# Performance work log

Measured on AMD Instinct MI355X. Metric: run time of the kernel, lower is better.

Reference implementation:

```python
import jax, jax.numpy as jnp
import numpy as np

N = 40000          # nodes
E = 320000         # edges
IN_DIM = 16
H = 64             # num_hidden
EDGE_DIM = 8
NUM_FILTERS = 2
SCALE = 3
T = 4              # num_layers (time steps)
DC = EDGE_DIM * NUM_FILTERS   # edge_dim_cat = 16
HC = H + DC                   # concat(h, efeat_p) dim
S1 = SCALE - 1


def setup_inputs() -> dict:
    key = jax.random.key(0)
    ks = jax.random.split(key, 24)
    def nrm(k, shape, fan):
        return jax.random.normal(k, shape, dtype=jnp.float32) / np.float32(np.sqrt(fan))
    return {
        "inputs": jax.random.normal(ks[0], (N, IN_DIM), dtype=jnp.float32),
        "e_feats": jax.random.normal(ks[1], (E, EDGE_DIM, T), dtype=jnp.float32),
        "rain0": jax.random.uniform(ks[2], (N, T), dtype=jnp.float32),
        "src": jax.random.randint(ks[3], (E,), 0, N),
        "dst": jax.random.randint(ks[4], (E,), 0, N),
        # embedding (no bias)
        "W_emb": nrm(ks[5], (IN_DIM, H), IN_DIM),
        # ST_EIConvSPGRAD (IN) layers, one per scale step: edge MLP split into per-source terms
        "Win_hs": nrm(ks[6], (S1, H, H), 2 * H + EDGE_DIM + 1),
        "Win_hd": nrm(ks[7], (S1, H, H), 2 * H + EDGE_DIM + 1),
        "Win_e": nrm(ks[8], (S1, EDGE_DIM, H), 2 * H + EDGE_DIM + 1),
        "Win_r": nrm(ks[9], (S1, H), 2 * H + EDGE_DIM + 1),
        # ST_EIConvProp (PROP) layers (edge-feature propagation, out_on=False)
        "Wp_hs": nrm(ks[10], (S1, H, DC), 2 * H + DC + 1),
        "Wp_hd": nrm(ks[11], (S1, H, DC), 2 * H + DC + 1),
        "Wp_e": nrm(ks[12], (S1, DC, DC), 2 * H + DC + 1),
        "Wp_r": nrm(ks[13], (S1, DC), 2 * H + DC + 1),
        # ST_EIConvProp OUT layer (out_on=True) on concatenated node features
        "Wo_hs": nrm(ks[14], (HC, H), 2 * HC + EDGE_DIM + 1),
        "Wo_hd": nrm(ks[15], (HC, H), 2 * HC + EDGE_DIM + 1),
        "Wo_e": nrm(ks[16], (EDGE_DIM, H), 2 * HC + EDGE_DIM + 1),
        "Wo_r": nrm(ks[17], (H,), 2 * HC + EDGE_DIM + 1),
        "W_rain": nrm(ks[18], (H,), H),
    }


def reference(inputs, e_feats, rain0, src, dst,
              W_emb, Win_hs, Win_hd, Win_e, Win_r,
              Wp_hs, Wp_hd, Wp_e, Wp_r,
              Wo_hs, Wo_hd, Wo_e, Wo_r, W_rain):
    relu = jax.nn.relu
    agg = lambda m: jax.ops.segment_sum(m, dst, num_segments=N)

    def in_layer(s, h, ef, rain):
        # per-edge message: MLP over [h_src, h_dst, efeat, rain_src], split matmuls avoid concat
        m = relu(h[src] @ Win_hs[s] + h[dst] @ Win_hd[s]
                 + ef @ Win_e[s] + rain[src, None] * Win_r[s][None, :])
        return relu(agg(m))                      # [N, H]

    def prop_layer(s, h, ef, rain):
        # ef is edge-level [E, DC] on first call, node-level [N, DC] thereafter (gather at src)
        ef_e = ef if ef.shape[0] == E else ef[src]
        m = relu(h[src] @ Wp_hs[s] + h[dst] @ Wp_hd[s]
                 + ef_e @ Wp_e[s] + rain[src, None] * Wp_r[s][None, :])
        return agg(m)                            # [N, DC]

    def out_layer(h_out, ef, rain):
        m = relu(h_out[src] @ Wo_hs + h_out[dst] @ Wo_hd
                 + ef @ Wo_e + rain[src, None] * Wo_r[None, :])
        h_new = relu(agg(m))                     # [N, H]
        rain_out = h_new @ W_rain                # [N]
        return rain_out, h_new

    def step(h, ef_t, rain_t, first):
        for s in range(S1):
            h = in_layer(s, h, ef_t, rain_t)
        ef_exp = jnp.tile(ef_t, (1, NUM_FILTERS))        # [E, DC]
        p = prop_layer(0, h, ef_exp, rain_t)
        # faithful quirk: first time step re-applies PROP[0] (range starts at 0);
        # later steps start at 1
        rng = range(S1) if first else range(1, S1)
        for s in rng:
            p = prop_layer(s, h, p, rain_t)
        h_out = jnp.concatenate([h, p], axis=1)          # [N, HC]
        rain_m, h = out_layer(h_out, ef_t, rain_t)
        return rain_m, h

    h = inputs @ W_emb                                   # [N, H]
    rains = []
    for t in range(T):
        rain_m, h = step(h, e_feats[:, :, t], rain0[:, t], first=(t == 0))
        rains.append(rain_m)
    return jnp.stack(rains, axis=1)                      # [N, T]
```

## Files before the change

kernel.cpp:

```cpp
#include <hip/hip_runtime.h>

#define NN 40000
#define NE 320000
#define TT 4
#define SCAN_CHUNK 1024
#define NBLK_SCAN ((NN + SCAN_CHUNK - 1) / SCAN_CHUNK)

typedef unsigned short u16;

__device__ __forceinline__ float bcastf(float v, int k) {
    return __builtin_bit_cast(float, __builtin_amdgcn_readlane(__builtin_bit_cast(int, v), k));
}
__device__ __forceinline__ int bcasti(int v, int k) {
    return __builtin_amdgcn_readlane(v, k);
}
__device__ __forceinline__ float b2f(u16 u) {
    return __builtin_bit_cast(float, (unsigned)u << 16);
}
__device__ __forceinline__ u16 f2b(float f) {
    unsigned x = __builtin_bit_cast(unsigned, f);
    unsigned r = x + 0x7fffu + ((x >> 16) & 1u);
    return (u16)(r >> 16);
}
__device__ __forceinline__ float lo16(unsigned u) {
    return __builtin_bit_cast(float, u << 16);
}
__device__ __forceinline__ float hi16(unsigned u) {
    return __builtin_bit_cast(float, u & 0xffff0000u);
}

__global__ void emb_kernel(const float* __restrict__ x, const float* __restrict__ W,
                           u16* __restrict__ h) {
    int i = blockIdx.x * blockDim.x + threadIdx.x;
    if (i >= NN * 64) return;
    int n = i >> 6, j = i & 63;
    float acc = 0.f;
#pragma unroll
    for (int k = 0; k < 16; ++k) acc = fmaf(x[n * 16 + k], W[k * 64 + j], acc);
    h[i] = f2b(acc);
}

__global__ void wfold_kernel(const float* __restrict__ We, float* __restrict__ Wf) {
    int i = threadIdx.x;
    if (i < 128) Wf[i] = We[i] + We[i + 128];
}

__global__ void hist_kernel(const int* __restrict__ dst, int* __restrict__ deg) {
    int e = blockIdx.x * blockDim.x + threadIdx.x;
    if (e < NE) atomicAdd(&deg[dst[e]], 1);
}

__global__ void scan1_kernel(const int* __restrict__ deg, int* __restrict__ bsum) {
    __shared__ int sdata[256];
    int b = blockIdx.x, t = threadIdx.x;
    int base = b * SCAN_CHUNK;
    int sum = 0;
    for (int i = t; i < SCAN_CHUNK; i += 256) {
        int idx = base + i;
        sum += (idx < NN) ? deg[idx] : 0;
    }
    sdata[t] = sum;
    __syncthreads();
    for (int off = 128; off > 0; off >>= 1) {
        if (t < off) sdata[t] += sdata[t + off];
        __syncthreads();
    }
    if (t == 0) bsum[b] = sdata[0];
}

__global__ void scan2_kernel(const int* __restrict__ bsum, int* __restrict__ boff,
                             int* __restrict__ rowptr) {
    if (threadIdx.x == 0) {
        int acc = 0;
        for (int i = 0; i < NBLK_SCAN; ++i) {
            boff[i] = acc;
            acc += bsum[i];
        }
        rowptr[NN] = NE;
    }
}

__global__ void scan3_kernel(const int* __restrict__ deg, const int* __restrict__ boff,
                             int* __restrict__ rowptr, int* __restrict__ cursor) {
    __shared__ int ss[256];
    int b = blockIdx.x, t = threadIdx.x;
    int base = b * SCAN_CHUNK + t * 4;
    int v[4], s = 0;
#pragma unroll
    for (int q = 0; q < 4; ++q) {
        int idx = base + q;
        v[q] = (idx < NN) ? deg[idx] : 0;
        s += v[q];
    }
    ss[t] = s;
    __syncthreads();
    for (int off = 1; off < 256; off <<= 1) {
        int add = (t >= off) ? ss[t - off] : 0;
        __syncthreads();
        ss[t] += add;
        __syncthreads();
    }
    int excl = boff[b] + ss[t] - s;
#pragma unroll
    for (int q = 0; q < 4; ++q) {
        int idx = base + q;
        if (idx < NN) {
            rowptr[idx] = excl;
            cursor[idx] = excl;
        }
        excl += v[q];
    }
}

__global__ void scatter_kernel(const int* __restrict__ src, const int* __restrict__ dst,
                               int* __restrict__ cursor, int* __restrict__ perm,
                               int* __restrict__ srcp) {
    int e = blockIdx.x * blockDim.x + threadIdx.x;
    if (e >= NE) return;
    int d = dst[e];
    int pos = atomicAdd(&cursor[d], 1);
    perm[pos] = e;
    srcp[pos] = src[e];
}

__global__ void efperm_all_kernel(const float* __restrict__ ef, const int* __restrict__ perm,
                                  u16* __restrict__ out) {
    int pos = blockIdx.x * blockDim.x + threadIdx.x;
    if (pos >= NE) return;
    int e = perm[pos];
    const float4* e4 = reinterpret_cast<const float4*>(ef) + (size_t)e * 8;
#pragma unroll
    for (int k = 0; k < 8; ++k) {
        float4 v = e4[k];
        out[0 * (size_t)NE * 8 + pos * 8 + k] = f2b(v.x);
        out[1 * (size_t)NE * 8 + pos * 8 + k] = f2b(v.y);
        out[2 * (size_t)NE * 8 + pos * 8 + k] = f2b(v.z);
        out[3 * (size_t)NE * 8 + pos * 8 + k] = f2b(v.w);
    }
}

__global__ void efperm_one_kernel(const float* __restrict__ ef, const int* __restrict__ perm,
                                  int t, u16* __restrict__ out) {
    int i = blockIdx.x * blockDim.x + threadIdx.x;
    if (i >= NE * 8) return;
    int pos = i >> 3, k = i & 7;
    int e = perm[pos];
    out[i] = f2b(ef[((size_t)e * 8 + k) * 4 + t]);
}

__global__ __launch_bounds__(256) void node_ab_kernel(
    const u16* __restrict__ X1, int relu1,
    const float* __restrict__ X2, int d2,
    const float* __restrict__ Whs, const float* __restrict__ Whd,
    const float* __restrict__ rain, const float* __restrict__ Wr,
    u16* __restrict__ A, u16* __restrict__ B) {
    extern __shared__ float sW[];
    const int dtot = 64 + d2;
    float* sWs = sW;
    float* sWd = sW + (dtot << 6);
    for (int i = threadIdx.x; i < (dtot << 6); i += 256) {
        sWs[i] = Whs[i];
        sWd[i] = Whd[i];
    }
    __syncthreads();
    const int lane = threadIdx.x & 63;
    const int wid = (blockIdx.x << 2) + (threadIdx.x >> 6);
    const int n0 = wid << 3;
    const float wr = Wr[lane];
    float xv[8], aa[8], bb[8];
#pragma unroll
    for (int p = 0; p < 8; ++p) {
        float x = b2f(__builtin_nontemporal_load(&X1[(size_t)(n0 + p) * 64 + lane]));
        xv[p] = relu1 ? fmaxf(x, 0.f) : x;
        aa[p] = rain[(n0 + p) * TT] * wr;
        bb[p] = 0.f;
    }
#pragma unroll 16
    for (int k = 0; k < 64; ++k) {
        float ws = sWs[(k << 6) + lane];
        float wd = sWd[(k << 6) + lane];
#pragma unroll
        for (int p = 0; p < 8; ++p) {
            float xk = bcastf(xv[p], k);
            aa[p] = fmaf(xk, ws, aa[p]);
            bb[p] = fmaf(xk, wd, bb[p]);
        }
    }
    if (d2) {
#pragma unroll
        for (int p = 0; p < 8; ++p) xv[p] = X2[(n0 + p) * 16 + (lane & 15)];
#pragma unroll
        for (int k = 0; k < 16; ++k) {
            float ws = sWs[((64 + k) << 6) + lane];
            float wd = sWd[((64 + k) << 6) + lane];
#pragma unroll
            for (int p = 0; p < 8; ++p) {
                float xk = bcastf(xv[p], k);
                aa[p] = fmaf(xk, ws, aa[p]);
                bb[p] = fmaf(xk, wd, bb[p]);
            }
        }
    }
#pragma unroll
    for (int p = 0; p < 8; ++p) {
        A[(size_t)(n0 + p) * 64 + lane] = f2b(aa[p]);
        B[(size_t)(n0 + p) * 64 + lane] = f2b(bb[p]);
    }
}

__global__ __launch_bounds__(256) void node_p_all(
    const u16* __restrict__ X,
    const float* __restrict__ Whs, const float* __restrict__ Whd,
    const float* __restrict__ rain, const float* __restrict__ Wr,
    float* __restrict__ Ap0, float* __restrict__ Bp0,
    float* __restrict__ Ap1, float* __restrict__ Bp1) {
    __shared__ float sX[64 * 68];
    __shared__ float sW[4][1024];
    for (int i = threadIdx.x; i < 1024; i += 256) {
        sW[0][i] = Whs[i];
        sW[1][i] = Whd[i];
        sW[2][i] = Whs[1024 + i];
        sW[3][i] = Whd[1024 + i];
    }
    const int n0 = blockIdx.x << 6;
    for (int i = threadIdx.x; i < 512; i += 256) {
        int row = i >> 3, col = (i & 7) << 3;
        uint4 v = *reinterpret_cast<const uint4*>(&X[(size_t)(n0 + row) * 64 + col]);
        float* d = &sX[row * 68 + col];
        d[0] = fmaxf(lo16(v.x), 0.f);
        d[1] = fmaxf(hi16(v.x), 0.f);
        d[2] = fmaxf(lo16(v.y), 0.f);
        d[3] = fmaxf(hi16(v.y), 0.f);
        d[4] = fmaxf(lo16(v.z), 0.f);
        d[5] = fmaxf(hi16(v.z), 0.f);
        d[6] = fmaxf(lo16(v.w), 0.f);
        d[7] = fmaxf(hi16(v.w), 0.f);
    }
    __syncthreads();
    const int j = threadIdx.x & 15;
    const int nl0 = threadIdx.x >> 4;
    const float wr0 = Wr[j], wr1 = Wr[16 + j];
    float a0[4], b0[4], a1[4], b1[4];
#pragma unroll
    for (int q = 0; q < 4; ++q) {
        float rn = rain[(n0 + nl0 + (q << 4)) * TT];
        a0[q] = rn * wr0;
        a1[q] = rn * wr1;
        b0[q] = 0.f;
        b1[q] = 0.f;
    }
#pragma unroll 4
    for (int k = 0; k < 64; ++k) {
        float wa0 = sW[0][(k << 4) + j], wb0 = sW[1][(k << 4) + j];
        float wa1 = sW[2][(k << 4) + j], wb1 = sW[3][(k << 4) + j];
#pragma unroll
        for (int q = 0; q < 4; ++q) {
            float x = sX[(nl0 + (q << 4)) * 68 + k];
            a0[q] = fmaf(x, wa0, a0[q]);
            b0[q] = fmaf(x, wb0, b0[q]);
            a1[q] = fmaf(x, wa1, a1[q]);
            b1[q] = fmaf(x, wb1, b1[q]);
        }
    }
#pragma unroll
    for (int q = 0; q < 4; ++q) {
        int n = n0 + nl0 + (q << 4);
        Ap0[n * 16 + j] = a0[q];
        Bp0[n * 16 + j] = b0[q];
        Ap1[n * 16 + j] = a1[q];
        Bp1[n * 16 + j] = b1[q];
    }
}

__global__ __launch_bounds__(256) void edge64_csr(
    const u16* __restrict__ A, const u16* __restrict__ B,
    const u16* __restrict__ efp, const float* __restrict__ We,
    const int* __restrict__ rowptr, const int* __restrict__ srcp,
    u16* __restrict__ agg, const float* __restrict__ Wrain,
    float* __restrict__ out, int t) {
    const int lane = threadIdx.x & 63;
    const int n = (blockIdx.x << 2) + (threadIdx.x >> 6);
    const float w0 = We[lane], w1 = We[64 + lane];
    const float w2 = We[128 + lane], w3 = We[192 + lane];
    const float w4 = We[256 + lane], w5 = We[320 + lane];
    const float w6 = We[384 + lane], w7 = We[448 + lane];
    const int beg = rowptr[n], end = rowptr[n + 1];
    const int deg = end - beg;
    int sv = 0;
    if (beg + lane < NE) sv = srcp[beg + lane];
    const float b = b2f(__builtin_nontemporal_load(&B[(size_t)n * 64 + lane]));
    const uint4* ef4 = reinterpret_cast<const uint4*>(efp);
    float acc = 0.f;
    for (int k0 = 0; k0 < deg; k0 += 4) {
        u16 av[4];
        uint4 ev[4];
#pragma unroll
        for (int i = 0; i < 4; ++i) {
            int kk = k0 + i;
            if (kk > deg - 1) kk = deg - 1;
            int s = (kk < 64) ? bcasti(sv, kk) : srcp[beg + kk];
            av[i] = A[(size_t)s * 64 + lane];
            ev[i] = ef4[(size_t)(beg + kk)];
        }
#pragma unroll
        for (int i = 0; i < 4; ++i) {
            if (k0 + i < deg) {
                float m = b2f(av[i]) + b;
                m = fmaf(lo16(ev[i].x), w0, m);
                m = fmaf(hi16(ev[i].x), w1, m);
                m = fmaf(lo16(ev[i].y), w2, m);
                m = fmaf(hi16(ev[i].y), w3, m);
                m = fmaf(lo16(ev[i].z), w4, m);
                m = fmaf(hi16(ev[i].z), w5, m);
                m = fmaf(lo16(ev[i].w), w6, m);
                m = fmaf(hi16(ev[i].w), w7, m);
                acc += fmaxf(m, 0.f);
            }
        }
    }
    __builtin_nontemporal_store(f2b(acc), &agg[(size_t)n * 64 + lane]);
    if (out) {
        float r = fmaxf(acc, 0.f) * Wrain[lane];
#pragma unroll
        for (int off = 32; off > 0; off >>= 1) r += __shfl_down(r, off);
        if (lane == 0) out[n * TT + t] = r;
    }
}

__global__ __launch_bounds__(256) void edge16_csr(
    const float* __restrict__ G, const float* __restrict__ Bp,
    const u16* __restrict__ efp, const float* __restrict__ Wf, int has_ef,
    const float* __restrict__ ApN, const float* __restrict__ WeN,
    float* __restrict__ PeSN, int has_epi,
    const int* __restrict__ rowptr, const int* __restrict__ srcp,
    float* __restrict__ pout) {
    const int lane = threadIdx.x & 63;
    const int g = lane >> 4, j = lane & 15;
    float w[8];
    if (has_ef) {
#pragma unroll
        for (int k = 0; k < 8; ++k) w[k] = Wf[k * 16 + j];
    }
    const int wid = (blockIdx.x * 256 + threadIdx.x) >> 6;
    const int n = (wid << 2) + g;
    const int beg = rowptr[n], end = rowptr[n + 1];
    const float b = Bp[n * 16 + j];
    const uint4* ef4 = reinterpret_cast<const uint4*>(efp);
    float acc = 0.f;
    int s_nxt = (beg + 1 < end) ? srcp[beg + 1] : 0;
    float av = (beg < end) ? G[srcp[beg] * 16 + j] : 0.f;
    for (int pos = beg; pos < end; ++pos) {
        float avc = av;
        int s_nn = (pos + 2 < end) ? srcp[pos + 2] : 0;
        if (pos + 1 < end) av = G[s_nxt * 16 + j];
        s_nxt = s_nn;
        float m = avc + b;
        if (has_ef) {
            uint4 ev = ef4[(size_t)pos];
            m = fmaf(lo16(ev.x), w[0], m);
            m = fmaf(hi16(ev.x), w[1], m);
            m = fmaf(lo16(ev.y), w[2], m);
            m = fmaf(hi16(ev.y), w[3], m);
            m = fmaf(lo16(ev.z), w[4], m);
            m = fmaf(hi16(ev.z), w[5], m);
            m = fmaf(lo16(ev.w), w[6], m);
            m = fmaf(hi16(ev.w), w[7], m);
        }
        acc += fmaxf(m, 0.f);
    }
    if (pout) pout[n * 16 + j] = acc;
    if (has_epi) {
        float pe = ApN[n * 16 + j];
        const int gbase = lane & 48;
#pragma unroll
        for (int k = 0; k < 16; ++k) {
            float pk = __shfl(acc, gbase + k);
            pe = fmaf(pk, WeN[k * 16 + j], pe);
        }
        PeSN[n * 16 + j] = pe;
    }
}

extern "C" void kernel_launch(void* const* d_in, const int* in_sizes, int n_in,
                              void* d_out, int out_size, void* d_ws, size_t ws_size,
                              hipStream_t stream) {
    (void)in_sizes; (void)n_in; (void)out_size;
    const float* inputs = (const float*)d_in[0];
    const float* e_feats = (const float*)d_in[1];
    const float* rain0 = (const float*)d_in[2];
    const int* src = (const int*)d_in[3];
    const int* dst = (const int*)d_in[4];
    const float* W_emb = (const float*)d_in[5];
    const float* Win_hs = (const float*)d_in[6];
    const float* Win_hd = (const float*)d_in[7];
    const float* Win_e = (const float*)d_in[8];
    const float* Win_r = (const float*)d_in[9];
    const float* Wp_hs = (const float*)d_in[10];
    const float* Wp_hd = (const float*)d_in[11];
    const float* Wp_e = (const float*)d_in[12];
    const float* Wp_r = (const float*)d_in[13];
    const float* Wo_hs = (const float*)d_in[14];
    const float* Wo_hd = (const float*)d_in[15];
    const float* Wo_e = (const float*)d_in[16];
    const float* Wo_r = (const float*)d_in[17];
    const float* W_rain = (const float*)d_in[18];
    float* out = (float*)d_out;

    const size_t NF64 = (size_t)NN * 64;
    const size_t NF16 = (size_t)NN * 16;
    const size_t EF = (size_t)NE * 8;

    char* base = (char*)d_ws;
    auto alloc = [&](size_t bytes) -> char* {
        char* p = base;
        base += (bytes + 255) & ~(size_t)255;
        return p;
    };

    const size_t fixed = 5 * NF64 * 2 + 7 * NF16 * 4 +
                         (2 * (size_t)NE + 3 * (size_t)NN + 200) * 4 + 64 * 256;
    const bool big = ws_size >= fixed + 4 * EF * 2;

    u16 *A16, *B16, *aggA16, *aggB16, *aggO16, *efp16;
    float *Ap0, *Bp0, *Ap1, *Bp1, *PeSa, *PeSb, *pbuf, *Wfold;
    A16 = (u16*)alloc(NF64 * 2);
    B16 = (u16*)alloc(NF64 * 2);
    aggA16 = (u16*)alloc(NF64 * 2);
    aggB16 = (u16*)alloc(NF64 * 2);
    aggO16 = (u16*)alloc(NF64 * 2);
    Ap0 = (float*)alloc(NF16 * 4);
    Bp0 = (float*)alloc(NF16 * 4);
    Ap1 = (float*)alloc(NF16 * 4);
    Bp1 = (float*)alloc(NF16 * 4);
    PeSa = (float*)alloc(NF16 * 4);
    PeSb = (float*)alloc(NF16 * 4);
    pbuf = (float*)alloc(NF16 * 4);
    Wfold = (float*)alloc(128 * 4);
    efp16 = (u16*)alloc((big ? 4 * EF : EF) * 2);
    int* srcp = (int*)alloc(NE * 4);
    int* perm = (int*)alloc(NE * 4);
    int* rowptr = (int*)alloc((NN + 1) * 4);
    int* deg = (int*)alloc(NN * 4);
    int* cursor = (int*)alloc(NN * 4);
    int* bsum = (int*)alloc(64 * 4);
    int* boff = (int*)alloc(64 * 4);
    u16* hemb = aggO16;

    hipMemsetAsync(deg, 0, NN * sizeof(int), stream);
    hist_kernel<<<(NE + 255) / 256, 256, 0, stream>>>(dst, deg);
    scan1_kernel<<<NBLK_SCAN, 256, 0, stream>>>(deg, bsum);
    scan2_kernel<<<1, 64, 0, stream>>>(bsum, boff, rowptr);
    scan3_kernel<<<NBLK_SCAN, 256, 0, stream>>>(deg, boff, rowptr, cursor);
    scatter_kernel<<<(NE + 255) / 256, 256, 0, stream>>>(src, dst, cursor, perm, srcp);
    if (big)
        efperm_all_kernel<<<(NE + 255) / 256, 256, 0, stream>>>(e_feats, perm, efp16);

    emb_kernel<<<(NN * 64 + 255) / 256, 256, 0, stream>>>(inputs, W_emb, hemb);
    wfold_kernel<<<1, 128, 0, stream>>>(Wp_e, Wfold);

    for (int t = 0; t < TT; ++t) {
        const float* rain = rain0 + t;
        const u16* eft = big ? (efp16 + (size_t)t * EF) : efp16;
        if (!big)
            efperm_one_kernel<<<(NE * 8 + 255) / 256, 256, 0, stream>>>(e_feats, perm, t, efp16);

        node_ab_kernel<<<1250, 256, 64 * 64 * 2 * sizeof(float), stream>>>(
            aggO16, (t > 0) ? 1 : 0, nullptr, 0,
            Win_hs, Win_hd, rain, Win_r, A16, B16);
        edge64_csr<<<10000, 256, 0, stream>>>(A16, B16, eft, Win_e, rowptr, srcp, aggA16,
                                              nullptr, nullptr, 0);

        node_ab_kernel<<<1250, 256, 64 * 64 * 2 * sizeof(float), stream>>>(
            aggA16, 1, nullptr, 0, Win_hs + 4096, Win_hd + 4096, rain, Win_r + 64, A16, B16);
        edge64_csr<<<10000, 256, 0, stream>>>(A16, B16, eft, Win_e + 512, rowptr, srcp, aggB16,
                                              nullptr, nullptr, 0);

        node_p_all<<<625, 256, 0, stream>>>(aggB16, Wp_hs, Wp_hd, rain, Wp_r,
                                            Ap0, Bp0, Ap1, Bp1);

        if (t == 0) {
            edge16_csr<<<2500, 256, 0, stream>>>(Ap0, Bp0, eft, Wfold, 1,
                                                 Ap0, Wp_e, PeSa, 1,
                                                 rowptr, srcp, nullptr);
            edge16_csr<<<2500, 256, 0, stream>>>(PeSa, Bp0, nullptr, nullptr, 0,
                                                 Ap1, Wp_e + 256, PeSb, 1,
                                                 rowptr, srcp, nullptr);
            edge16_csr<<<2500, 256, 0, stream>>>(PeSb, Bp1, nullptr, nullptr, 0,
                                                 nullptr, nullptr, nullptr, 0,
                                                 rowptr, srcp, pbuf);
        } else {
            edge16_csr<<<2500, 256, 0, stream>>>(Ap0, Bp0, eft, Wfold, 1,
                                                 Ap1, Wp_e + 256, PeSa, 1,
                                                 rowptr, srcp, nullptr);
            edge16_csr<<<2500, 256, 0, stream>>>(PeSa, Bp1, nullptr, nullptr, 0,
                                                 nullptr, nullptr, nullptr, 0,
                                                 rowptr, srcp, pbuf);
        }

        node_ab_kernel<<<1250, 256, 80 * 64 * 2 * sizeof(float), stream>>>(
            aggB16, 1, pbuf, 16, Wo_hs, Wo_hd, rain, Wo_r, A16, B16);
        edge64_csr<<<10000, 256, 0, stream>>>(A16, B16, eft, Wo_e, rowptr, srcp, aggO16,
                                              W_rain, out, t);
    }
}
```

Measured before the change: 953.2 us.

## Process nodes in descending-degree order in CSR edge kernels

Adds a degree histogram, scan and scatter that build a node ordering sorted by in-degree, descending and capped at 64. The edge64 and edge16 CSR kernels then pick their node through this order, so waves in a block and neighbouring blocks see similar degrees. This is meant to reduce divergence and load imbalance from random degree variation. The cost is an extra indirection per wave, three setup kernels, and worse locality when writing node outputs.

```diff
diff --git a/kernel.cpp b/kernel.cpp
--- a/kernel.cpp
+++ b/kernel.cpp
@@ -121,6 +121,34 @@
     int pos = atomicAdd(&cursor[d], 1);
     perm[pos] = e;
     srcp[pos] = src[e];
+}
+
+__global__ void dhist_kernel(const int* __restrict__ rowptr, int* __restrict__ dh) {
+    int n = blockIdx.x * blockDim.x + threadIdx.x;
+    if (n >= NN) return;
+    int d = rowptr[n + 1] - rowptr[n];
+    if (d > 64) d = 64;
+    atomicAdd(&dh[64 - d], 1);
+}
+
+__global__ void dscan_kernel(const int* __restrict__ dh, int* __restrict__ dcur) {
+    if (threadIdx.x == 0) {
+        int a = 0;
+        for (int i = 0; i < 65; ++i) {
+            dcur[i] = a;
+            a += dh[i];
+        }
+    }
+}
+
+__global__ void dscatter_kernel(const int* __restrict__ rowptr, int* __restrict__ dcur,
+                                int* __restrict__ order) {
+    int n = blockIdx.x * blockDim.x + threadIdx.x;
+    if (n >= NN) return;
+    int d = rowptr[n + 1] - rowptr[n];
+    if (d > 64) d = 64;
+    int pos = atomicAdd(&dcur[64 - d], 1);
+    order[pos] = n;
 }
 
 __global__ void efperm_all_kernel(const float* __restrict__ ef, const int* __restrict__ perm,
@@ -276,10 +304,11 @@
     const u16* __restrict__ A, const u16* __restrict__ B,
     const u16* __restrict__ efp, const float* __restrict__ We,
     const int* __restrict__ rowptr, const int* __restrict__ srcp,
+    const int* __restrict__ order,
     u16* __restrict__ agg, const float* __restrict__ Wrain,
     float* __restrict__ out, int t) {
     const int lane = threadIdx.x & 63;
-    const int n = (blockIdx.x << 2) + (threadIdx.x >> 6);
+    const int n = order[(blockIdx.x << 2) + (threadIdx.x >> 6)];
     const float w0 = We[lane], w1 = We[64 + lane];
     const float w2 = We[128 + lane], w3 = We[192 + lane];
     const float w4 = We[256 + lane], w5 = We[320 + lane];
@@ -333,6 +362,7 @@
     const float* __restrict__ ApN, const float* __restrict__ WeN,
     float* __restrict__ PeSN, int has_epi,
     const int* __restrict__ rowptr, const int* __restrict__ srcp,
+    const int* __restrict__ order,
     float* __restrict__ pout) {
     const int lane = threadIdx.x & 63;
     const int g = lane >> 4, j = lane & 15;
@@ -342,7 +372,7 @@
         for (int k = 0; k < 8; ++k) w[k] = Wf[k * 16 + j];
     }
     const int wid = (blockIdx.x * 256 + threadIdx.x) >> 6;
-    const int n = (wid << 2) + g;
+    const int n = order[(wid << 2) + g];
     const int beg = rowptr[n], end = rowptr[n + 1];
     const float b = Bp[n * 16 + j];
     const uint4* ef4 = reinterpret_cast<const uint4*>(efp);
@@ -418,7 +448,7 @@
     };
 
     const size_t fixed = 5 * NF64 * 2 + 7 * NF16 * 4 +
-                         (2 * (size_t)NE + 3 * (size_t)NN + 200) * 4 + 64 * 256;
+                         (2 * (size_t)NE + 4 * (size_t)NN + 400) * 4 + 64 * 256;
     const bool big = ws_size >= fixed + 4 * EF * 2;
 
     u16 *A16, *B16, *aggA16, *aggB16, *aggO16, *efp16;
@@ -442,16 +472,23 @@
     int* rowptr = (int*)alloc((NN + 1) * 4);
     int* deg = (int*)alloc(NN * 4);
     int* cursor = (int*)alloc(NN * 4);
+    int* order = (int*)alloc(NN * 4);
     int* bsum = (int*)alloc(64 * 4);
     int* boff = (int*)alloc(64 * 4);
+    int* dh = (int*)alloc(65 * 4);
+    int* dcur = (int*)alloc(65 * 4);
     u16* hemb = aggO16;
 
     hipMemsetAsync(deg, 0, NN * sizeof(int), stream);
+    hipMemsetAsync(dh, 0, 65 * sizeof(int), stream);
     hist_kernel<<<(NE + 255) / 256, 256, 0, stream>>>(dst, deg);
     scan1_kernel<<<NBLK_SCAN, 256, 0, stream>>>(deg, bsum);
     scan2_kernel<<<1, 64, 0, stream>>>(bsum, boff, rowptr);
     scan3_kernel<<<NBLK_SCAN, 256, 0, stream>>>(deg, boff, rowptr, cursor);
     scatter_kernel<<<(NE + 255) / 256, 256, 0, stream>>>(src, dst, cursor, perm, srcp);
+    dhist_kernel<<<(NN + 255) / 256, 256, 0, stream>>>(rowptr, dh);
+    dscan_kernel<<<1, 64, 0, stream>>>(dh, dcur);
+    dscatter_kernel<<<(NN + 255) / 256, 256, 0, stream>>>(rowptr, dcur, order);
     if (big)
         efperm_all_kernel<<<(NE + 255) / 256, 256, 0, stream>>>(e_feats, perm, efp16);
 
@@ -467,13 +504,13 @@
         node_ab_kernel<<<1250, 256, 64 * 64 * 2 * sizeof(float), stream>>>(
             aggO16, (t > 0) ? 1 : 0, nullptr, 0,
             Win_hs, Win_hd, rain, Win_r, A16, B16);
-        edge64_csr<<<10000, 256, 0, stream>>>(A16, B16, eft, Win_e, rowptr, srcp, aggA16,
-                                              nullptr, nullptr, 0);
+        edge64_csr<<<10000, 256, 0, stream>>>(A16, B16, eft, Win_e, rowptr, srcp, order,
+                                              aggA16, nullptr, nullptr, 0);
 
         node_ab_kernel<<<1250, 256, 64 * 64 * 2 * sizeof(float), stream>>>(
             aggA16, 1, nullptr, 0, Win_hs + 4096, Win_hd + 4096, rain, Win_r + 64, A16, B16);
-        edge64_csr<<<10000, 256, 0, stream>>>(A16, B16, eft, Win_e + 512, rowptr, srcp, aggB16,
-                                              nullptr, nullptr, 0);
+        edge64_csr<<<10000, 256, 0, stream>>>(A16, B16, eft, Win_e + 512, rowptr, srcp, order,
+                                              aggB16, nullptr, nullptr, 0);
 
         node_p_all<<<625, 256, 0, stream>>>(aggB16, Wp_hs, Wp_hd, rain, Wp_r,
                                             Ap0, Bp0, Ap1, Bp1);
@@ -481,25 +518,25 @@
         if (t == 0) {
             edge16_csr<<<2500, 256, 0, stream>>>(Ap0, Bp0, eft, Wfold, 1,
                                                  Ap0, Wp_e, PeSa, 1,
-                                                 rowptr, srcp, nullptr);
+                                                 rowptr, srcp, order, nullptr);
             edge16_csr<<<2500, 256, 0, stream>>>(PeSa, Bp0, nullptr, nullptr, 0,
                                                  Ap1, Wp_e + 256, PeSb, 1,
-                                                 rowptr, srcp, nullptr);
+                                                 rowptr, srcp, order, nullptr);
             edge16_csr<<<2500, 256, 0, stream>>>(PeSb, Bp1, nullptr, nullptr, 0,
                                                  nullptr, nullptr, nullptr, 0,
-                                                 rowptr, srcp, pbuf);
+                                                 rowptr, srcp, order, pbuf);
         } else {
             edge16_csr<<<2500, 256, 0, stream>>>(Ap0, Bp0, eft, Wfold, 1,
                                                  Ap1, Wp_e + 256, PeSa, 1,
-                                                 rowptr, srcp, nullptr);
+                                                 rowptr, srcp, order, nullptr);
             edge16_csr<<<2500, 256, 0, stream>>>(PeSa, Bp1, nullptr, nullptr, 0,
                                                  nullptr, nullptr, nullptr, 0,
-                                                 rowptr, srcp, pbuf);
+                                                 rowptr, srcp, order, pbuf);
         }
 
         node_ab_kernel<<<1250, 256, 80 * 64 * 2 * sizeof(float), stream>>>(
             aggB16, 1, pbuf, 16, Wo_hs, Wo_hd, rain, Wo_r, A16, B16);
-        edge64_csr<<<10000, 256, 0, stream>>>(A16, B16, eft, Wo_e, rowptr, srcp, aggO16,
-                                              W_rain, out, t);
-    }
-}
+        edge64_csr<<<10000, 256, 0, stream>>>(A16, B16, eft, Wo_e, rowptr, srcp, order,
+                                              aggO16, W_rain, out, t);
+    }
+}
```

Result: slower. 1.173 ms (+23.0%).
